# Performance work log

Hardware: AMD Instinct MI355X
Metric: run time of the kernel (lower is better)

The kernel has to match this reference:

```python
import jax, jax.numpy as jnp
import numpy as np

N = 50000
E = 800000
IN = 128
H = 128
C = 64
BN_EPS = 1e-5


def gcn_conv(x, W, b, src, dst, n_nodes):
    # GCNConv: add self-loops, symmetric normalization D^-1/2 (A+I) D^-1/2, linear, bias
    deg = jax.ops.segment_sum(jnp.ones_like(dst, dtype=x.dtype), dst, num_segments=n_nodes)
    dinv = jnp.where(deg > 0, jax.lax.rsqrt(deg), jnp.zeros_like(deg))
    norm = dinv[src] * dinv[dst]                      # [E+N]
    h = x @ W                                         # [N, out]
    agg = jax.ops.segment_sum(norm[:, None] * h[src], dst, num_segments=n_nodes)
    return agg + b


def batch_norm_eval(x, gamma, beta, mean, var):
    return gamma * (x - mean) * jax.lax.rsqrt(var + BN_EPS) + beta


def setup_inputs() -> dict:
    key = jax.random.key(0)
    ks = jax.random.split(key, 16)
    inp = {
        "x": jax.random.normal(ks[0], (N, IN), dtype=jnp.float32),
        "edge_index": jax.random.randint(ks[1], (2, E), 0, N, dtype=jnp.int64),
        "W1": jax.random.normal(ks[2], (IN, H), dtype=jnp.float32) / np.sqrt(IN),
        "b1": jnp.zeros((H,), dtype=jnp.float32),
        "g1": jnp.ones((H,), dtype=jnp.float32),
        "be1": jnp.zeros((H,), dtype=jnp.float32),
        "m1": jax.random.normal(ks[3], (H,), dtype=jnp.float32) * 0.1,
        "v1": jax.random.uniform(ks[4], (H,), dtype=jnp.float32, minval=0.5, maxval=1.5),
        "W2": jax.random.normal(ks[5], (H, H), dtype=jnp.float32) / np.sqrt(H),
        "b2": jnp.zeros((H,), dtype=jnp.float32),
        "g2": jnp.ones((H,), dtype=jnp.float32),
        "be2": jnp.zeros((H,), dtype=jnp.float32),
        "m2": jax.random.normal(ks[6], (H,), dtype=jnp.float32) * 0.1,
        "v2": jax.random.uniform(ks[7], (H,), dtype=jnp.float32, minval=0.5, maxval=1.5),
        "W3": jax.random.normal(ks[8], (H, C), dtype=jnp.float32) / np.sqrt(H),
        "b3": jnp.zeros((C,), dtype=jnp.float32),
    }
    return inp


def reference(x, edge_index, W1, b1, g1, be1, m1, v1, W2, b2, g2, be2, m2, v2, W3, b3):
    # add self loops once (shared across layers, GCNConv cached=True)
    loop = jnp.arange(N, dtype=edge_index.dtype)
    src = jnp.concatenate([edge_index[0], loop])
    dst = jnp.concatenate([edge_index[1], loop])

    h = gcn_conv(x, W1, b1, src, dst, N)
    h = jax.nn.relu(batch_norm_eval(h, g1, be1, m1, v1))  # eval mode: dropout is identity
    h = gcn_conv(h, W2, b2, src, dst, N)
    h = jax.nn.relu(batch_norm_eval(h, g2, be2, m2, v2))
    out = gcn_conv(h, W3, b3, src, dst, N)
    return out
```

## Files before the change

### kernel.cpp

```cpp
#include <hip/hip_runtime.h>


#define SCAN_CHUNK 1024
#define NCHUNK 256
#define BSHIFT 8
#define BWID 256
#define ECAP 8192

typedef __attribute__((ext_vector_type(8))) short bf16x8;
typedef __attribute__((ext_vector_type(4))) float f32x4;

__device__ __forceinline__ float blo(unsigned p) { return __uint_as_float(p << 16); }
__device__ __forceinline__ float bhi(unsigned p) { return __uint_as_float(p & 0xffff0000u); }
__device__ __forceinline__ unsigned short f2b(float f) {
  unsigned u = __float_as_uint(f);
  unsigned r = (u + 0x7fffu + ((u >> 16) & 1u)) >> 16;
  return (unsigned short)r;
}

__global__ void detect_dtype_kernel(const int* __restrict__ ei32, int* flag) {
  int t = threadIdx.x;
  int any = 0;
  for (int i = 2 * t + 1; i < 8192; i += 512) any |= (ei32[i] != 0);
  if (any) atomicOr(flag, 1);
}

__device__ __forceinline__ int edge_val(const int* ei32, const long long* ei64,
                                        int is32, int idx) {
  return is32 ? ei32[idx] : (int)ei64[idx];
}

__global__ void wprep_kernel(const float* __restrict__ W1, const float* __restrict__ W2,
                             const float* __restrict__ W3,
                             unsigned short* __restrict__ Wt1,
                             unsigned short* __restrict__ Wt2,
                             unsigned short* __restrict__ Wt3) {
  int i = blockIdx.x * 256 + threadIdx.x;
  if (i < 16384) {
    int k = i >> 7, c = i & 127;
    Wt1[c * 128 + k] = f2b(W1[i]);
  } else if (i < 32768) {
    int j = i - 16384; int k = j >> 7, c = j & 127;
    Wt2[c * 128 + k] = f2b(W2[j]);
  } else {
    int j = i - 32768;
    if (j < 8192) { int k = j >> 6, c = j & 63; Wt3[c * 128 + k] = f2b(W3[j]); }
  }
}

__global__ __launch_bounds__(256) void bin_hist_kernel(
    const int* __restrict__ ei32, const long long* __restrict__ ei64,
    const int* __restrict__ flag, int* __restrict__ counts, int E, int nbk) {
  __shared__ int hist[BWID];
  int k = blockIdx.x, t = threadIdx.x;
  hist[t] = 0;
  __syncthreads();
  int is32 = *flag;
  int CH = (E + NCHUNK - 1) / NCHUNK;
  int e0 = k * CH, e1 = min(e0 + CH, E);
  for (int e = e0 + t; e < e1; e += 256) {
    int d = edge_val(ei32, ei64, is32, E + e);
    atomicAdd(&hist[d >> BSHIFT], 1);
  }
  __syncthreads();
  if (t < nbk) counts[t * NCHUNK + k] = hist[t];
}

__global__ __launch_bounds__(256) void scan_partial_kernel(
    const int* __restrict__ src, int* __restrict__ bsum, int n) {
  __shared__ int wsum[4];
  int b = blockIdx.x, t = threadIdx.x;
  int lane = t & 63, wv = t >> 6;
  int i0 = b * SCAN_CHUNK + t * 4;
  int4 d4 = make_int4(0, 0, 0, 0);
  if (i0 + 3 < n) d4 = *(const int4*)&src[i0];
  else {
    if (i0 < n) d4.x = src[i0];
    if (i0 + 1 < n) d4.y = src[i0 + 1];
    if (i0 + 2 < n) d4.z = src[i0 + 2];
  }
  int s = d4.x + d4.y + d4.z + d4.w;
#pragma unroll
  for (int off = 32; off; off >>= 1) s += __shfl_xor(s, off);
  if (lane == 0) wsum[wv] = s;
  __syncthreads();
  if (t == 0) bsum[b] = wsum[0] + wsum[1] + wsum[2] + wsum[3];
}

__global__ void scan_bsum_kernel(const int* __restrict__ bsum,
                                 int* __restrict__ boff,
                                 int* __restrict__ outp, int nb, int n) {
  int t = threadIdx.x;
  int v = (t < nb) ? bsum[t] : 0;
  int inc = v;
#pragma unroll
  for (int off = 1; off < 64; off <<= 1) {
    int u = __shfl_up(inc, off);
    if (t >= off) inc += u;
  }
  boff[t] = inc - v;
  if (t == 63) outp[n] = inc;
}

template <bool DEG>
__global__ __launch_bounds__(256) void scan_write_kernel(
    const int* __restrict__ src, const int* __restrict__ boff,
    int* __restrict__ outp, float* __restrict__ dinv, int n) {
  __shared__ int woff[4];
  int b = blockIdx.x, t = threadIdx.x;
  int lane = t & 63, wv = t >> 6;
  int i0 = b * SCAN_CHUNK + t * 4;
  int4 d4 = make_int4(0, 0, 0, 0);
  if (i0 + 3 < n) d4 = *(const int4*)&src[i0];
  else {
    if (i0 < n) d4.x = src[i0];
    if (i0 + 1 < n) d4.y = src[i0 + 1];
    if (i0 + 2 < n) d4.z = src[i0 + 2];
  }
  int tsum = d4.x + d4.y + d4.z + d4.w;
  int inc = tsum;
#pragma unroll
  for (int off = 1; off < 64; off <<= 1) {
    int u = __shfl_up(inc, off);
    if (lane >= off) inc += u;
  }
  if (lane == 63) woff[wv] = inc;
  __syncthreads();
  if (t == 0) {
    int r = 0;
#pragma unroll
    for (int w = 0; w < 4; ++w) { int sw = woff[w]; woff[w] = r; r += sw; }
  }
  __syncthreads();
  int p = inc - tsum + woff[wv] + boff[b];
  int dg[4] = {d4.x, d4.y, d4.z, d4.w};
#pragma unroll
  for (int j = 0; j < 4; ++j) {
    int i = i0 + j;
    if (i < n) {
      outp[i] = p;
      if constexpr (DEG) dinv[i] = rsqrtf((float)(dg[j] + 1));
      p += dg[j];
    }
  }
}

__global__ __launch_bounds__(256) void bin_scatter_kernel(
    const int* __restrict__ ei32, const long long* __restrict__ ei64,
    const int* __restrict__ flag, const int* __restrict__ offs,
    unsigned* __restrict__ pairs, int E, int nbk) {
  __shared__ int cur[BWID];
  int k = blockIdx.x, t = threadIdx.x;
  if (t < nbk) cur[t] = offs[t * NCHUNK + k];
  __syncthreads();
  int is32 = *flag;
  int CH = (E + NCHUNK - 1) / NCHUNK;
  int e0 = k * CH, e1 = min(e0 + CH, E);
  for (int e = e0 + t; e < e1; e += 256) {
    int s = edge_val(ei32, ei64, is32, e);
    int d = edge_val(ei32, ei64, is32, E + e);
    int pos = atomicAdd(&cur[d >> BSHIFT], 1);
    pairs[pos] = (unsigned)s | ((unsigned)(d & (BWID - 1)) << 20);
  }
}

__global__ __launch_bounds__(256) void bucket_deg_kernel(
    const unsigned* __restrict__ pairs, const int* __restrict__ offs,
    int* __restrict__ degi, int E, int n, int nbk) {
  __shared__ int deg[BWID];
  int b = blockIdx.x, t = threadIdx.x;
  deg[t] = 0;
  __syncthreads();
  int base = offs[b * NCHUNK];
  int end = (b + 1 < nbk) ? offs[(b + 1) * NCHUNK] : E;
  for (int i = base + t; i < end; i += 256) {
    atomicAdd(&deg[pairs[i] >> 20], 1);
  }
  __syncthreads();
  int idx = b * BWID + t;
  if (idx < n) degi[idx] = deg[t];
}

__global__ __launch_bounds__(256) void bucket_col_kernel(
    const unsigned* __restrict__ pairs, const int* __restrict__ offs,
    const int* __restrict__ rowptr, int* __restrict__ col,
    int E, int n, int nbk) {
  __shared__ int cur[BWID];
  __shared__ int stage[ECAP];
  int b = blockIdx.x, t = threadIdx.x;
  int rowbase = rowptr[b * BWID];
  int idx = b * BWID + t;
  cur[t] = ((idx < n) ? rowptr[idx] : rowptr[n]) - rowbase;
  __syncthreads();
  int base = offs[b * NCHUNK];
  int end = (b + 1 < nbk) ? offs[(b + 1) * NCHUNK] : E;
  for (int i = base + t; i < end; i += 256) {
    unsigned p = pairs[i];
    int pos = atomicAdd(&cur[p >> 20], 1);
    if (pos < ECAP) stage[pos] = (int)(p & 0xFFFFFu);
  }
  __syncthreads();
  int hi = b * BWID + BWID;
  int nE = ((hi < n) ? rowptr[hi] : rowptr[n]) - rowbase;
  for (int i = t; i < nE; i += 256) col[rowbase + i] = stage[i];
}

template <int HOUT, int ABF16>
__global__ __launch_bounds__(256) void mgemm_kernel(
    const void* __restrict__ Ain, const unsigned short* __restrict__ Wt,
    unsigned short* __restrict__ Y, int n) {
  constexpr int NT = HOUT;
  __shared__ unsigned char AsB[64 * 256];
  __shared__ unsigned char BsB[NT * 256];
  int t = threadIdx.x;
  int row0 = blockIdx.x * 64;

  if constexpr (ABF16) {
    const unsigned short* A = (const unsigned short*)Ain;
#pragma unroll
    for (int jj = 0; jj < 4; ++jj) {
      int f = t + 256 * jj; int r = f >> 4, kq = f & 15;
      uint4 v = make_uint4(0, 0, 0, 0);
      if (row0 + r < n) v = *(const uint4*)&A[(size_t)(row0 + r) * 128 + kq * 8];
      *(uint4*)&AsB[r * 256 + ((kq * 16) ^ ((r & 15) << 4))] = v;
    }
  } else {
    const float* A = (const float*)Ain;
#pragma unroll
    for (int jj = 0; jj < 8; ++jj) {
      int f = t + 256 * jj; int r = f >> 5, kq = f & 31;
      float4 v = make_float4(0.f, 0.f, 0.f, 0.f);
      if (row0 + r < n) v = *(const float4*)&A[(size_t)(row0 + r) * 128 + kq * 4];
      unsigned two0 = (unsigned)f2b(v.x) | ((unsigned)f2b(v.y) << 16);
      unsigned two1 = (unsigned)f2b(v.z) | ((unsigned)f2b(v.w) << 16);
      uint2 o = make_uint2(two0, two1);
      *(uint2*)&AsB[r * 256 + ((kq * 8) ^ ((r & 15) << 4))] = o;
    }
  }
#pragma unroll
  for (int jj = 0; jj < NT / 16; ++jj) {
    int f = t + 256 * jj; int c = f >> 4, kq = f & 15;
    uint4 v = *(const uint4*)&Wt[(size_t)c * 128 + kq * 8];
    *(uint4*)&BsB[c * 256 + ((kq * 16) ^ ((c & 15) << 4))] = v;
  }
  __syncthreads();

  int l = t & 63, wid = t >> 6;
  constexpr int WC = NT / 2;
  constexpr int NI = WC / 16;
  int wr = (wid >> 1) * 32, wc = (wid & 1) * WC;
  int lr = l & 15, lk = (l >> 4) * 16;

  f32x4 acc[2][NI] = {};
#pragma unroll
  for (int ks = 0; ks < 4; ++ks) {
    bf16x8 a[2], b[NI];
#pragma unroll
    for (int mi = 0; mi < 2; ++mi) {
      int r = wr + mi * 16 + lr;
      a[mi] = *(const bf16x8*)&AsB[r * 256 + ((ks * 64 + lk) ^ ((r & 15) << 4))];
    }
#pragma unroll
    for (int ni = 0; ni < NI; ++ni) {
      int c = wc + ni * 16 + lr;
      b[ni] = *(const bf16x8*)&BsB[c * 256 + ((ks * 64 + lk) ^ ((c & 15) << 4))];
    }
#pragma unroll
    for (int mi = 0; mi < 2; ++mi)
#pragma unroll
      for (int ni = 0; ni < NI; ++ni)
        acc[mi][ni] = __builtin_amdgcn_mfma_f32_16x16x32_bf16(a[mi], b[ni],
                                                              acc[mi][ni], 0, 0, 0);
  }

#pragma unroll
  for (int mi = 0; mi < 2; ++mi) {
#pragma unroll
    for (int reg = 0; reg < 4; ++reg) {
      int gr = row0 + wr + mi * 16 + (l >> 4) * 4 + reg;
      if (gr < n) {
#pragma unroll
        for (int ni = 0; ni < NI; ++ni) {
          int gc = wc + ni * 16 + lr;
          Y[(size_t)gr * HOUT + gc] = f2b(acc[mi][ni][reg]);
        }
      }
    }
  }
}

template <int HOUT, bool BN, bool OUTBF>
__global__ __launch_bounds__(256) void agg_kernel(
    const unsigned short* __restrict__ h, const int* __restrict__ rowptr,
    const int* __restrict__ col, const float* __restrict__ dinv,
    const float* __restrict__ bias,
    const float* __restrict__ g, const float* __restrict__ be,
    const float* __restrict__ m, const float* __restrict__ v,
    void* __restrict__ out, int n_nodes) {
  int wid = (blockIdx.x * blockDim.x + threadIdx.x) >> 6;
  int lane = threadIdx.x & 63;
  const unsigned* hu = (const unsigned*)h;

  constexpr int RW = HOUT / 2;
  int n, sub;
  if (HOUT == 128) {
    n = wid; sub = lane;
  } else {
    n = wid * 2 + (lane >> 5); sub = lane & 31;
  }
  if (n >= n_nodes) return;

  float dn = dinv[n];
  int beg = rowptr[n], end = rowptr[n + 1];
  unsigned selfp = hu[(size_t)n * RW + sub];
  float acc0 = dn * dn * blo(selfp);
  float acc1 = dn * dn * bhi(selfp);

  int j = beg;
  for (; j + 7 < end; j += 8) {
    int s[8]; float w[8]; unsigned p[8];
#pragma unroll
    for (int u = 0; u < 8; ++u) s[u] = col[j + u];
#pragma unroll
    for (int u = 0; u < 8; ++u) p[u] = hu[(size_t)s[u] * RW + sub];
#pragma unroll
    for (int u = 0; u < 8; ++u) w[u] = dn * dinv[s[u]];
#pragma unroll
    for (int u = 0; u < 8; ++u) {
      acc0 = fmaf(w[u], blo(p[u]), acc0);
      acc1 = fmaf(w[u], bhi(p[u]), acc1);
    }
  }
  for (; j + 3 < end; j += 4) {
    int s[4]; float w[4]; unsigned p[4];
#pragma unroll
    for (int u = 0; u < 4; ++u) s[u] = col[j + u];
#pragma unroll
    for (int u = 0; u < 4; ++u) p[u] = hu[(size_t)s[u] * RW + sub];
#pragma unroll
    for (int u = 0; u < 4; ++u) w[u] = dn * dinv[s[u]];
#pragma unroll
    for (int u = 0; u < 4; ++u) {
      acc0 = fmaf(w[u], blo(p[u]), acc0);
      acc1 = fmaf(w[u], bhi(p[u]), acc1);
    }
  }
  for (; j < end; ++j) {
    int s = col[j];
    float w = dn * dinv[s];
    unsigned p = hu[(size_t)s * RW + sub];
    acc0 = fmaf(w, blo(p), acc0);
    acc1 = fmaf(w, bhi(p), acc1);
  }

  int c0 = sub * 2;
  float y0 = acc0 + bias[c0];
  float y1 = acc1 + bias[c0 + 1];
  if constexpr (BN) {
    y0 = g[c0] * (y0 - m[c0]) * rsqrtf(v[c0] + 1e-5f) + be[c0];
    y1 = g[c0 + 1] * (y1 - m[c0 + 1]) * rsqrtf(v[c0 + 1] + 1e-5f) + be[c0 + 1];
    y0 = fmaxf(y0, 0.f);
    y1 = fmaxf(y1, 0.f);
  }
  if constexpr (OUTBF) {
    unsigned pk = (unsigned)f2b(y0) | ((unsigned)f2b(y1) << 16);
    ((unsigned*)out)[(size_t)n * RW + sub] = pk;
  } else {
    float2 o; o.x = y0; o.y = y1;
    *(float2*)&((float*)out)[(size_t)n * HOUT + c0] = o;
  }
}

extern "C" void kernel_launch(void* const* d_in, const int* in_sizes, int n_in,
                              void* d_out, int out_size, void* d_ws, size_t ws_size,
                              hipStream_t stream) {
  const float* x = (const float*)d_in[0];
  const int* ei32 = (const int*)d_in[1];
  const long long* ei64 = (const long long*)d_in[1];
  const float* W1 = (const float*)d_in[2];
  const float* b1 = (const float*)d_in[3];
  const float* g1 = (const float*)d_in[4];
  const float* be1 = (const float*)d_in[5];
  const float* m1 = (const float*)d_in[6];
  const float* v1 = (const float*)d_in[7];
  const float* W2 = (const float*)d_in[8];
  const float* b2 = (const float*)d_in[9];
  const float* g2 = (const float*)d_in[10];
  const float* be2 = (const float*)d_in[11];
  const float* m2 = (const float*)d_in[12];
  const float* v2 = (const float*)d_in[13];
  const float* W3 = (const float*)d_in[14];
  const float* b3 = (const float*)d_in[15];

  const int N = in_sizes[0] / 128;
  const int E = in_sizes[1] / 2;
  const int NBK = (N + BWID - 1) / BWID;
  const int NC = NBK * NCHUNK;

  char* ws = (char*)d_ws;
  size_t off = 0;
  auto alloc = [&](size_t bytes) -> void* {
    void* p = ws + off;
    off = (off + bytes + 255) & ~(size_t)255;
    return p;
  };
  float* dinv = (float*)alloc((size_t)N * 4);
  int* rowptr = (int*)alloc((size_t)(N + 1) * 4);
  int* degi = (int*)alloc((size_t)N * 4);
  int* counts = (int*)alloc((size_t)(NC + 1) * 4);
  int* offs = (int*)alloc((size_t)(NC + 1) * 4);
  int* col = (int*)alloc((size_t)E * 4);
  unsigned* pairs = (unsigned*)alloc((size_t)E * 4);
  int* flag = (int*)alloc(256);
  int* bsum = (int*)alloc(64 * 4);
  int* boff = (int*)alloc(64 * 4);
  unsigned short* wt1 = (unsigned short*)alloc(128 * 128 * 2);
  unsigned short* wt2 = (unsigned short*)alloc(128 * 128 * 2);
  unsigned short* wt3 = (unsigned short*)alloc(128 * 64 * 2);
  unsigned short* hbuf = (unsigned short*)alloc((size_t)N * 128 * 2);
  unsigned short* ybuf = (unsigned short*)alloc((size_t)N * 128 * 2);
  (void)ws_size;

  hipMemsetAsync(flag, 0, 4, stream);
  detect_dtype_kernel<<<1, 256, 0, stream>>>(ei32, flag);
  wprep_kernel<<<160, 256, 0, stream>>>(W1, W2, W3, wt1, wt2, wt3);

  bin_hist_kernel<<<NCHUNK, 256, 0, stream>>>(ei32, ei64, flag, counts, E, NBK);
  int nbC = (NC + SCAN_CHUNK - 1) / SCAN_CHUNK;
  scan_partial_kernel<<<nbC, 256, 0, stream>>>(counts, bsum, NC);
  scan_bsum_kernel<<<1, 64, 0, stream>>>(bsum, boff, offs, nbC, NC);
  scan_write_kernel<false><<<nbC, 256, 0, stream>>>(counts, boff, offs, nullptr, NC);
  bin_scatter_kernel<<<NCHUNK, 256, 0, stream>>>(ei32, ei64, flag, offs, pairs, E, NBK);
  bucket_deg_kernel<<<NBK, 256, 0, stream>>>(pairs, offs, degi, E, N, NBK);
  int nbN = (N + SCAN_CHUNK - 1) / SCAN_CHUNK;
  scan_partial_kernel<<<nbN, 256, 0, stream>>>(degi, bsum, N);
  scan_bsum_kernel<<<1, 64, 0, stream>>>(bsum, boff, rowptr, nbN, N);
  scan_write_kernel<true><<<nbN, 256, 0, stream>>>(degi, boff, rowptr, dinv, N);
  bucket_col_kernel<<<NBK, 256, 0, stream>>>(pairs, offs, rowptr, col, E, N, NBK);

  int gb = (N + 63) / 64;
  int ab128 = (N + 3) / 4;
  int ab64 = (N + 7) / 8;

  mgemm_kernel<128, 0><<<gb, 256, 0, stream>>>(x, wt1, hbuf, N);
  agg_kernel<128, true, true><<<ab128, 256, 0, stream>>>(hbuf, rowptr, col, dinv,
                                                         b1, g1, be1, m1, v1, ybuf, N);
  mgemm_kernel<128, 1><<<gb, 256, 0, stream>>>(ybuf, wt2, hbuf, N);
  agg_kernel<128, true, true><<<ab128, 256, 0, stream>>>(hbuf, rowptr, col, dinv,
                                                         b2, g2, be2, m2, v2, ybuf, N);
  mgemm_kernel<64, 1><<<gb, 256, 0, stream>>>(ybuf, wt3, hbuf, N);
  agg_kernel<64, false, false><<<ab64, 256, 0, stream>>>(hbuf, rowptr, col, dinv,
                                                         b3, nullptr, nullptr, nullptr,
                                                         nullptr, d_out, N);
}
```

Measured before the change: 181.1 us.

## Precompute edge weights into CSR, split neighbors across wave halves, fold BN params, drop small kernels

The CSR column array now stores (source, normalized weight) pairs, so aggregation no longer gathers dinv per edge. Each wave processes one node with lanes split into phases that handle interleaved edges, using 8-byte feature loads and a shuffle reduction at the end; the 64-wide layer now also uses one node per wave. BatchNorm and bias are folded into precomputed scale/shift vectors. The dtype-detection kernel, the memset and the block-sum scan kernels are removed by doing that work inline, which cuts launches but makes each scan block redo a small prefix scan and doubles the column-array traffic.

```diff
diff --git a/kernel.cpp b/kernel.cpp
--- a/kernel.cpp
+++ b/kernel.cpp
@@ -18,23 +18,19 @@
   return (unsigned short)r;
 }
 
-__global__ void detect_dtype_kernel(const int* __restrict__ ei32, int* flag) {
-  int t = threadIdx.x;
-  int any = 0;
-  for (int i = 2 * t + 1; i < 8192; i += 512) any |= (ei32[i] != 0);
-  if (any) atomicOr(flag, 1);
-}
-
-__device__ __forceinline__ int edge_val(const int* ei32, const long long* ei64,
-                                        int is32, int idx) {
-  return is32 ? ei32[idx] : (int)ei64[idx];
-}
-
 __global__ void wprep_kernel(const float* __restrict__ W1, const float* __restrict__ W2,
                              const float* __restrict__ W3,
+                             const float* __restrict__ b1, const float* __restrict__ g1,
+                             const float* __restrict__ be1, const float* __restrict__ m1,
+                             const float* __restrict__ v1,
+                             const float* __restrict__ b2, const float* __restrict__ g2,
+                             const float* __restrict__ be2, const float* __restrict__ m2,
+                             const float* __restrict__ v2,
                              unsigned short* __restrict__ Wt1,
                              unsigned short* __restrict__ Wt2,
-                             unsigned short* __restrict__ Wt3) {
+                             unsigned short* __restrict__ Wt3,
+                             float* __restrict__ sc1, float* __restrict__ sh1,
+                             float* __restrict__ sc2, float* __restrict__ sh2) {
   int i = blockIdx.x * 256 + threadIdx.x;
   if (i < 16384) {
     int k = i >> 7, c = i & 127;
@@ -42,24 +38,36 @@
   } else if (i < 32768) {
     int j = i - 16384; int k = j >> 7, c = j & 127;
     Wt2[c * 128 + k] = f2b(W2[j]);
-  } else {
-    int j = i - 32768;
-    if (j < 8192) { int k = j >> 6, c = j & 63; Wt3[c * 128 + k] = f2b(W3[j]); }
+  } else if (i < 40960) {
+    int j = i - 32768; int k = j >> 6, c = j & 63;
+    Wt3[c * 128 + k] = f2b(W3[j]);
+  } else if (i < 41088) {
+    int c = i - 40960;
+    float s = g1[c] * rsqrtf(v1[c] + 1e-5f);
+    sc1[c] = s; sh1[c] = (b1[c] - m1[c]) * s + be1[c];
+  } else if (i < 41216) {
+    int c = i - 41088;
+    float s = g2[c] * rsqrtf(v2[c] + 1e-5f);
+    sc2[c] = s; sh2[c] = (b2[c] - m2[c]) * s + be2[c];
   }
 }
 
 __global__ __launch_bounds__(256) void bin_hist_kernel(
     const int* __restrict__ ei32, const long long* __restrict__ ei64,
-    const int* __restrict__ flag, int* __restrict__ counts, int E, int nbk) {
+    int* __restrict__ counts, int E, int nbk) {
   __shared__ int hist[BWID];
+  __shared__ int s_is32;
   int k = blockIdx.x, t = threadIdx.x;
   hist[t] = 0;
-  __syncthreads();
-  int is32 = *flag;
+  if (t == 0) s_is32 = 0;
   int CH = (E + NCHUNK - 1) / NCHUNK;
   int e0 = k * CH, e1 = min(e0 + CH, E);
+  __syncthreads();
+  if (t < 64 && e0 + t < E && ei32[2 * (e0 + t) + 1] != 0) atomicOr(&s_is32, 1);
+  __syncthreads();
+  int is32 = s_is32;
   for (int e = e0 + t; e < e1; e += 256) {
-    int d = edge_val(ei32, ei64, is32, E + e);
+    int d = is32 ? ei32[E + e] : (int)ei64[E + e];
     atomicAdd(&hist[d >> BSHIFT], 1);
   }
   __syncthreads();
@@ -87,28 +95,25 @@
   if (t == 0) bsum[b] = wsum[0] + wsum[1] + wsum[2] + wsum[3];
 }
 
-__global__ void scan_bsum_kernel(const int* __restrict__ bsum,
-                                 int* __restrict__ boff,
-                                 int* __restrict__ outp, int nb, int n) {
-  int t = threadIdx.x;
-  int v = (t < nb) ? bsum[t] : 0;
-  int inc = v;
-#pragma unroll
-  for (int off = 1; off < 64; off <<= 1) {
-    int u = __shfl_up(inc, off);
-    if (t >= off) inc += u;
-  }
-  boff[t] = inc - v;
-  if (t == 63) outp[n] = inc;
-}
-
 template <bool DEG>
 __global__ __launch_bounds__(256) void scan_write_kernel(
-    const int* __restrict__ src, const int* __restrict__ boff,
-    int* __restrict__ outp, float* __restrict__ dinv, int n) {
+    const int* __restrict__ src, const int* __restrict__ bsum,
+    int* __restrict__ outp, float* __restrict__ dinv, int n, int nb) {
   __shared__ int woff[4];
+  __shared__ int s_boff;
   int b = blockIdx.x, t = threadIdx.x;
   int lane = t & 63, wv = t >> 6;
+  if (t < 64) {
+    int v = (t < nb) ? bsum[t] : 0;
+    int ic = v;
+#pragma unroll
+    for (int off = 1; off < 64; off <<= 1) {
+      int u = __shfl_up(ic, off);
+      if (t >= off) ic += u;
+    }
+    if (t == b) s_boff = ic - v;
+    if (b == nb - 1 && t == 63) outp[n] = ic;
+  }
   int i0 = b * SCAN_CHUNK + t * 4;
   int4 d4 = make_int4(0, 0, 0, 0);
   if (i0 + 3 < n) d4 = *(const int4*)&src[i0];
@@ -132,7 +137,7 @@
     for (int w = 0; w < 4; ++w) { int sw = woff[w]; woff[w] = r; r += sw; }
   }
   __syncthreads();
-  int p = inc - tsum + woff[wv] + boff[b];
+  int p = inc - tsum + woff[wv] + s_boff;
   int dg[4] = {d4.x, d4.y, d4.z, d4.w};
 #pragma unroll
   for (int j = 0; j < 4; ++j) {
@@ -147,18 +152,22 @@
 
 __global__ __launch_bounds__(256) void bin_scatter_kernel(
     const int* __restrict__ ei32, const long long* __restrict__ ei64,
-    const int* __restrict__ flag, const int* __restrict__ offs,
-    unsigned* __restrict__ pairs, int E, int nbk) {
+    const int* __restrict__ offs, unsigned* __restrict__ pairs, int E, int nbk) {
   __shared__ int cur[BWID];
+  __shared__ int s_is32;
   int k = blockIdx.x, t = threadIdx.x;
   if (t < nbk) cur[t] = offs[t * NCHUNK + k];
-  __syncthreads();
-  int is32 = *flag;
+  if (t == 0) s_is32 = 0;
   int CH = (E + NCHUNK - 1) / NCHUNK;
   int e0 = k * CH, e1 = min(e0 + CH, E);
+  __syncthreads();
+  if (t < 64 && e0 + t < E && ei32[2 * (e0 + t) + 1] != 0) atomicOr(&s_is32, 1);
+  __syncthreads();
+  int is32 = s_is32;
   for (int e = e0 + t; e < e1; e += 256) {
-    int s = edge_val(ei32, ei64, is32, e);
-    int d = edge_val(ei32, ei64, is32, E + e);
+    int s, d;
+    if (is32) { s = ei32[e]; d = ei32[E + e]; }
+    else      { s = (int)ei64[e]; d = (int)ei64[E + e]; }
     int pos = atomicAdd(&cur[d >> BSHIFT], 1);
     pairs[pos] = (unsigned)s | ((unsigned)(d & (BWID - 1)) << 20);
   }
@@ -183,26 +192,32 @@
 
 __global__ __launch_bounds__(256) void bucket_col_kernel(
     const unsigned* __restrict__ pairs, const int* __restrict__ offs,
-    const int* __restrict__ rowptr, int* __restrict__ col,
-    int E, int n, int nbk) {
+    const int* __restrict__ rowptr, const float* __restrict__ dinv,
+    uint2* __restrict__ cw, int E, int n, int nbk) {
   __shared__ int cur[BWID];
-  __shared__ int stage[ECAP];
+  __shared__ float dsl[BWID];
+  __shared__ int stage_s[ECAP];
+  __shared__ float stage_w[ECAP];
   int b = blockIdx.x, t = threadIdx.x;
   int rowbase = rowptr[b * BWID];
   int idx = b * BWID + t;
   cur[t] = ((idx < n) ? rowptr[idx] : rowptr[n]) - rowbase;
+  dsl[t] = (idx < n) ? dinv[idx] : 0.f;
   __syncthreads();
   int base = offs[b * NCHUNK];
   int end = (b + 1 < nbk) ? offs[(b + 1) * NCHUNK] : E;
   for (int i = base + t; i < end; i += 256) {
     unsigned p = pairs[i];
-    int pos = atomicAdd(&cur[p >> 20], 1);
-    if (pos < ECAP) stage[pos] = (int)(p & 0xFFFFFu);
+    int s = (int)(p & 0xFFFFFu);
+    int dl = (int)(p >> 20);
+    int pos = atomicAdd(&cur[dl], 1);
+    if (pos < ECAP) { stage_s[pos] = s; stage_w[pos] = dinv[s] * dsl[dl]; }
   }
   __syncthreads();
   int hi = b * BWID + BWID;
   int nE = ((hi < n) ? rowptr[hi] : rowptr[n]) - rowbase;
-  for (int i = t; i < nE; i += 256) col[rowbase + i] = stage[i];
+  for (int i = t; i < nE; i += 256)
+    cw[rowbase + i] = make_uint2((unsigned)stage_s[i], __float_as_uint(stage_w[i]));
 }
 
 template <int HOUT, int ABF16>
@@ -292,82 +307,81 @@
 template <int HOUT, bool BN, bool OUTBF>
 __global__ __launch_bounds__(256) void agg_kernel(
     const unsigned short* __restrict__ h, const int* __restrict__ rowptr,
-    const int* __restrict__ col, const float* __restrict__ dinv,
-    const float* __restrict__ bias,
-    const float* __restrict__ g, const float* __restrict__ be,
-    const float* __restrict__ m, const float* __restrict__ v,
+    const uint2* __restrict__ cw, const float* __restrict__ dinv,
+    const float* __restrict__ sc, const float* __restrict__ sh,
     void* __restrict__ out, int n_nodes) {
-  int wid = (blockIdx.x * blockDim.x + threadIdx.x) >> 6;
+  int n = (blockIdx.x * blockDim.x + threadIdx.x) >> 6;
+  if (n >= n_nodes) return;
   int lane = threadIdx.x & 63;
-  const unsigned* hu = (const unsigned*)h;
-
-  constexpr int RW = HOUT / 2;
-  int n, sub;
-  if (HOUT == 128) {
-    n = wid; sub = lane;
-  } else {
-    n = wid * 2 + (lane >> 5); sub = lane & 31;
-  }
-  if (n >= n_nodes) return;
+  const uint2* hu2 = (const uint2*)h;
+  constexpr int RW2 = HOUT / 4;
+  constexpr int NPH = (HOUT == 128) ? 2 : 4;
+  constexpr int GL = 64 / NPH;
+  int phase = lane / GL;
+  int sub = lane & (GL - 1);
 
   float dn = dinv[n];
   int beg = rowptr[n], end = rowptr[n + 1];
-  unsigned selfp = hu[(size_t)n * RW + sub];
-  float acc0 = dn * dn * blo(selfp);
-  float acc1 = dn * dn * bhi(selfp);
-
-  int j = beg;
-  for (; j + 7 < end; j += 8) {
-    int s[8]; float w[8]; unsigned p[8];
-#pragma unroll
-    for (int u = 0; u < 8; ++u) s[u] = col[j + u];
-#pragma unroll
-    for (int u = 0; u < 8; ++u) p[u] = hu[(size_t)s[u] * RW + sub];
-#pragma unroll
-    for (int u = 0; u < 8; ++u) w[u] = dn * dinv[s[u]];
-#pragma unroll
-    for (int u = 0; u < 8; ++u) {
-      acc0 = fmaf(w[u], blo(p[u]), acc0);
-      acc1 = fmaf(w[u], bhi(p[u]), acc1);
-    }
-  }
-  for (; j + 3 < end; j += 4) {
-    int s[4]; float w[4]; unsigned p[4];
-#pragma unroll
-    for (int u = 0; u < 4; ++u) s[u] = col[j + u];
-#pragma unroll
-    for (int u = 0; u < 4; ++u) p[u] = hu[(size_t)s[u] * RW + sub];
-#pragma unroll
-    for (int u = 0; u < 4; ++u) w[u] = dn * dinv[s[u]];
-#pragma unroll
-    for (int u = 0; u < 4; ++u) {
-      acc0 = fmaf(w[u], blo(p[u]), acc0);
-      acc1 = fmaf(w[u], bhi(p[u]), acc1);
-    }
-  }
-  for (; j < end; ++j) {
-    int s = col[j];
-    float w = dn * dinv[s];
-    unsigned p = hu[(size_t)s * RW + sub];
-    acc0 = fmaf(w, blo(p), acc0);
-    acc1 = fmaf(w, bhi(p), acc1);
-  }
-
-  int c0 = sub * 2;
-  float y0 = acc0 + bias[c0];
-  float y1 = acc1 + bias[c0 + 1];
+  float a0 = 0.f, a1 = 0.f, a2 = 0.f, a3 = 0.f;
+  if (phase == 0) {
+    uint2 sp = hu2[(size_t)n * RW2 + sub];
+    float sw = dn * dn;
+    a0 = sw * blo(sp.x); a1 = sw * bhi(sp.x);
+    a2 = sw * blo(sp.y); a3 = sw * bhi(sp.y);
+  }
+
+  int j = beg + phase;
+  for (; j + 3 * NPH < end; j += 4 * NPH) {
+    uint2 e0 = cw[j], e1 = cw[j + NPH], e2 = cw[j + 2 * NPH], e3 = cw[j + 3 * NPH];
+    uint2 h0 = hu2[(size_t)e0.x * RW2 + sub];
+    uint2 h1 = hu2[(size_t)e1.x * RW2 + sub];
+    uint2 h2 = hu2[(size_t)e2.x * RW2 + sub];
+    uint2 h3 = hu2[(size_t)e3.x * RW2 + sub];
+    float w0 = __uint_as_float(e0.y), w1 = __uint_as_float(e1.y);
+    float w2 = __uint_as_float(e2.y), w3 = __uint_as_float(e3.y);
+    a0 = fmaf(w0, blo(h0.x), a0); a1 = fmaf(w0, bhi(h0.x), a1);
+    a2 = fmaf(w0, blo(h0.y), a2); a3 = fmaf(w0, bhi(h0.y), a3);
+    a0 = fmaf(w1, blo(h1.x), a0); a1 = fmaf(w1, bhi(h1.x), a1);
+    a2 = fmaf(w1, blo(h1.y), a2); a3 = fmaf(w1, bhi(h1.y), a3);
+    a0 = fmaf(w2, blo(h2.x), a0); a1 = fmaf(w2, bhi(h2.x), a1);
+    a2 = fmaf(w2, blo(h2.y), a2); a3 = fmaf(w2, bhi(h2.y), a3);
+    a0 = fmaf(w3, blo(h3.x), a0); a1 = fmaf(w3, bhi(h3.x), a1);
+    a2 = fmaf(w3, blo(h3.y), a2); a3 = fmaf(w3, bhi(h3.y), a3);
+  }
+  for (; j < end; j += NPH) {
+    uint2 e = cw[j];
+    uint2 hv = hu2[(size_t)e.x * RW2 + sub];
+    float w = __uint_as_float(e.y);
+    a0 = fmaf(w, blo(hv.x), a0); a1 = fmaf(w, bhi(hv.x), a1);
+    a2 = fmaf(w, blo(hv.y), a2); a3 = fmaf(w, bhi(hv.y), a3);
+  }
+
+  a0 += __shfl_xor(a0, 32); a1 += __shfl_xor(a1, 32);
+  a2 += __shfl_xor(a2, 32); a3 += __shfl_xor(a3, 32);
+  if constexpr (NPH == 4) {
+    a0 += __shfl_xor(a0, 16); a1 += __shfl_xor(a1, 16);
+    a2 += __shfl_xor(a2, 16); a3 += __shfl_xor(a3, 16);
+  }
+  if (phase != 0) return;
+
+  int c0 = sub * 4;
+  float y0, y1, y2, y3;
   if constexpr (BN) {
-    y0 = g[c0] * (y0 - m[c0]) * rsqrtf(v[c0] + 1e-5f) + be[c0];
-    y1 = g[c0 + 1] * (y1 - m[c0 + 1]) * rsqrtf(v[c0 + 1] + 1e-5f) + be[c0 + 1];
-    y0 = fmaxf(y0, 0.f);
-    y1 = fmaxf(y1, 0.f);
+    y0 = fmaxf(fmaf(a0, sc[c0], sh[c0]), 0.f);
+    y1 = fmaxf(fmaf(a1, sc[c0 + 1], sh[c0 + 1]), 0.f);
+    y2 = fmaxf(fmaf(a2, sc[c0 + 2], sh[c0 + 2]), 0.f);
+    y3 = fmaxf(fmaf(a3, sc[c0 + 3], sh[c0 + 3]), 0.f);
+  } else {
+    y0 = a0 + sh[c0]; y1 = a1 + sh[c0 + 1];
+    y2 = a2 + sh[c0 + 2]; y3 = a3 + sh[c0 + 3];
   }
   if constexpr (OUTBF) {
-    unsigned pk = (unsigned)f2b(y0) | ((unsigned)f2b(y1) << 16);
-    ((unsigned*)out)[(size_t)n * RW + sub] = pk;
+    unsigned p0 = (unsigned)f2b(y0) | ((unsigned)f2b(y1) << 16);
+    unsigned p1 = (unsigned)f2b(y2) | ((unsigned)f2b(y3) << 16);
+    ((uint2*)out)[(size_t)n * RW2 + sub] = make_uint2(p0, p1);
   } else {
-    float2 o; o.x = y0; o.y = y1;
-    *(float2*)&((float*)out)[(size_t)n * HOUT + c0] = o;
+    float4 o; o.x = y0; o.y = y1; o.z = y2; o.w = y3;
+    *(float4*)&((float*)out)[(size_t)n * HOUT + c0] = o;
   }
 }
 
@@ -409,47 +423,45 @@
   int* degi = (int*)alloc((size_t)N * 4);
   int* counts = (int*)alloc((size_t)(NC + 1) * 4);
   int* offs = (int*)alloc((size_t)(NC + 1) * 4);
-  int* col = (int*)alloc((size_t)E * 4);
+  uint2* cw = (uint2*)alloc((size_t)E * 8);
   unsigned* pairs = (unsigned*)alloc((size_t)E * 4);
-  int* flag = (int*)alloc(256);
   int* bsum = (int*)alloc(64 * 4);
-  int* boff = (int*)alloc(64 * 4);
   unsigned short* wt1 = (unsigned short*)alloc(128 * 128 * 2);
   unsigned short* wt2 = (unsigned short*)alloc(128 * 128 * 2);
   unsigned short* wt3 = (unsigned short*)alloc(128 * 64 * 2);
+  float* sc1 = (float*)alloc(128 * 4);
+  float* sh1 = (float*)alloc(128 * 4);
+  float* sc2 = (float*)alloc(128 * 4);
+  float* sh2 = (float*)alloc(128 * 4);
   unsigned short* hbuf = (unsigned short*)alloc((size_t)N * 128 * 2);
   unsigned short* ybuf = (unsigned short*)alloc((size_t)N * 128 * 2);
   (void)ws_size;
 
-  hipMemsetAsync(flag, 0, 4, stream);
-  detect_dtype_kernel<<<1, 256, 0, stream>>>(ei32, flag);
-  wprep_kernel<<<160, 256, 0, stream>>>(W1, W2, W3, wt1, wt2, wt3);
-
-  bin_hist_kernel<<<NCHUNK, 256, 0, stream>>>(ei32, ei64, flag, counts, E, NBK);
+  wprep_kernel<<<161, 256, 0, stream>>>(W1, W2, W3, b1, g1, be1, m1, v1,
+                                        b2, g2, be2, m2, v2,
+                                        wt1, wt2, wt3, sc1, sh1, sc2, sh2);
+
+  bin_hist_kernel<<<NCHUNK, 256, 0, stream>>>(ei32, ei64, counts, E, NBK);
   int nbC = (NC + SCAN_CHUNK - 1) / SCAN_CHUNK;
   scan_partial_kernel<<<nbC, 256, 0, stream>>>(counts, bsum, NC);
-  scan_bsum_kernel<<<1, 64, 0, stream>>>(bsum, boff, offs, nbC, NC);
-  scan_write_kernel<false><<<nbC, 256, 0, stream>>>(counts, boff, offs, nullptr, NC);
-  bin_scatter_kernel<<<NCHUNK, 256, 0, stream>>>(ei32, ei64, flag, offs, pairs, E, NBK);
+  scan_write_kernel<false><<<nbC, 256, 0, stream>>>(counts, bsum, offs, nullptr, NC, nbC);
+  bin_scatter_kernel<<<NCHUNK, 256, 0, stream>>>(ei32, ei64, offs, pairs, E, NBK);
   bucket_deg_kernel<<<NBK, 256, 0, stream>>>(pairs, offs, degi, E, N, NBK);
   int nbN = (N + SCAN_CHUNK - 1) / SCAN_CHUNK;
   scan_partial_kernel<<<nbN, 256, 0, stream>>>(degi, bsum, N);
-  scan_bsum_kernel<<<1, 64, 0, stream>>>(bsum, boff, rowptr, nbN, N);
-  scan_write_kernel<true><<<nbN, 256, 0, stream>>>(degi, boff, rowptr, dinv, N);
-  bucket_col_kernel<<<NBK, 256, 0, stream>>>(pairs, offs, rowptr, col, E, N, NBK);
+  scan_write_kernel<true><<<nbN, 256, 0, stream>>>(degi, bsum, rowptr, dinv, N, nbN);
+  bucket_col_kernel<<<NBK, 256, 0, stream>>>(pairs, offs, rowptr, dinv, cw, E, N, NBK);
 
   int gb = (N + 63) / 64;
-  int ab128 = (N + 3) / 4;
-  int ab64 = (N + 7) / 8;
+  int ab = (N + 3) / 4;
 
   mgemm_kernel<128, 0><<<gb, 256, 0, stream>>>(x, wt1, hbuf, N);
-  agg_kernel<128, true, true><<<ab128, 256, 0, stream>>>(hbuf, rowptr, col, dinv,
-                                                         b1, g1, be1, m1, v1, ybuf, N);
+  agg_kernel<128, true, true><<<ab, 256, 0, stream>>>(hbuf, rowptr, cw, dinv,
+                                                      sc1, sh1, ybuf, N);
   mgemm_kernel<128, 1><<<gb, 256, 0, stream>>>(ybuf, wt2, hbuf, N);
-  agg_kernel<128, true, true><<<ab128, 256, 0, stream>>>(hbuf, rowptr, col, dinv,
-                                                         b2, g2, be2, m2, v2, ybuf, N);
+  agg_kernel<128, true, true><<<ab, 256, 0, stream>>>(hbuf, rowptr, cw, dinv,
+                                                      sc2, sh2, ybuf, N);
   mgemm_kernel<64, 1><<<gb, 256, 0, stream>>>(ybuf, wt3, hbuf, N);
-  agg_kernel<64, false, false><<<ab64, 256, 0, stream>>>(hbuf, rowptr, col, dinv,
-                                                         b3, nullptr, nullptr, nullptr,
-                                                         nullptr, d_out, N);
-}
+  agg_kernel<64, false, false><<<ab, 256, 0, stream>>>(hbuf, rowptr, cw, dinv,
+                                                       nullptr, b3, d_out, N);
+}
```

After: 188.7 us. +4.2%, slower.
